# Performance work log

Measured on AMD Instinct MI355X. Metric: run time of the kernel, lower is better.

Reference implementation:

```python
import jax, jax.numpy as jnp
import numpy as np


def _conv(x, w):
    # stride-2, pad-1, 3x3 conv, NCHW activations, HWIO kernel
    return jax.lax.conv_general_dilated(
        x, w, (2, 2), [(1, 1), (1, 1)],
        dimension_numbers=('NCHW', 'HWIO', 'NCHW'))


def setup_inputs() -> dict:
    key = jax.random.key(0)
    ks = iter(jax.random.split(key, 40))
    def rn(shape, scale=1.0):
        return jax.random.normal(next(ks), shape, jnp.float32) * scale
    d = {}
    d['img'] = rn((64, 3, 128, 128))
    d['qst'] = rn((64, 128))
    d['conv_w0'] = rn((3, 3, 3, 24), 1.0 / np.sqrt(3 * 9))
    for i in (1, 2, 3):
        d['conv_w%d' % i] = rn((3, 3, 24, 24), 1.0 / np.sqrt(24 * 9))
    for i in range(4):
        d['bn_s%d' % i] = jax.random.uniform(next(ks), (24,), jnp.float32, 0.5, 1.5)
        d['bn_b%d' % i] = rn((24,), 0.1)
    d['g_w1'] = rn((180, 256), 1.0 / np.sqrt(180))
    d['g_b1'] = rn((256,), 0.01)
    for i in (2, 3, 4):
        d['g_w%d' % i] = rn((256, 256), 1.0 / np.sqrt(256))
        d['g_b%d' % i] = rn((256,), 0.01)
    d['f_w1'] = rn((256, 256), 1.0 / np.sqrt(256))
    d['f_b1'] = rn((256,), 0.01)
    d['f_w2'] = rn((256, 256), 1.0 / np.sqrt(256))
    d['f_b2'] = rn((256,), 0.01)
    d['cls_w'] = rn((256, 32), 1.0 / np.sqrt(256))
    d['cls_b'] = rn((32,), 0.01)
    return d


def reference(img, qst, conv_w0, conv_w1, conv_w2, conv_w3,
              bn_s0, bn_b0, bn_s1, bn_b1, bn_s2, bn_b2, bn_s3, bn_b3,
              g_w1, g_b1, g_w2, g_b2, g_w3, g_b3, g_w4, g_b4,
              f_w1, f_b1, f_w2, f_b2, cls_w, cls_b):
    x = img
    for w, s, b in ((conv_w0, bn_s0, bn_b0), (conv_w1, bn_s1, bn_b1),
                    (conv_w2, bn_s2, bn_b2), (conv_w3, bn_s3, bn_b3)):
        x = jax.nn.relu(_conv(x, w) * s[None, :, None, None] + b[None, :, None, None])
    N, C, H, W = x.shape  # [64, 24, 8, 8]
    # positional encoding: coords_x, coords_y in [-1,1]
    cx, cy = jnp.meshgrid(jnp.linspace(-1.0, 1.0, W), jnp.linspace(-1.0, 1.0, H))
    pos = jnp.broadcast_to(jnp.stack([cx, cy])[None], (N, 2, H, W)).astype(x.dtype)
    x = jnp.concatenate([x, pos], axis=1)              # [N, C+2, H, W]
    Cf = C + 2
    x = x.transpose(0, 2, 3, 1).reshape(N, H * W, Cf)  # [N, HW, 26]
    # RN_G first linear decomposed over concat([x_i, x_j, qst]) so the huge
    # [N, HW, HW, 2C+q] concat tensor is never materialized (same math).
    W1a, W1b, W1c = g_w1[:Cf], g_w1[Cf:2 * Cf], g_w1[2 * Cf:]
    hi = x @ W1a                      # [N, HW, 256]
    hj = x @ W1b                      # [N, HW, 256]
    hq = qst @ W1c + g_b1             # [N, 256]
    h = jax.nn.relu(hi[:, :, None, :] + hj[:, None, :, :] + hq[:, None, None, :])  # [N,HW,HW,256]
    h = jax.nn.relu(h @ g_w2 + g_b2)
    h = jax.nn.relu(h @ g_w3 + g_b3)
    h = jax.nn.relu(h @ g_w4 + g_b4)
    s = h.sum(axis=(1, 2))            # sum over all HW*HW pairs -> [N, 256]
    # RN_F (dropout is identity in eval mode)
    y = jax.nn.relu(s @ f_w1 + f_b1)
    y = jax.nn.relu(y @ f_w2 + f_b2)
    return jax.nn.log_softmax(y @ cls_w + cls_b, axis=1)
```

## Files before the change

### kernel.cpp

```cpp
#include <hip/hip_runtime.h>
#include <hip/hip_bf16.h>
#include <math.h>

typedef __bf16 bf16x8 __attribute__((ext_vector_type(8)));
typedef __bf16 bf16x4 __attribute__((ext_vector_type(4)));
typedef float  f32x4  __attribute__((ext_vector_type(4)));

#define LH 264

__device__ __host__ inline int fperm(int p) {
  return (p & 0xC0) | ((p & 0x0C) << 2) | ((p >> 2) & 0x0C) | (p & 3);
}

__global__ __launch_bounds__(256) void k1(const float* __restrict__ img, const float* __restrict__ w0,
    const float* __restrict__ bs0, const float* __restrict__ bb0,
    const float* __restrict__ g2, const float* __restrict__ g3, const float* __restrict__ g4,
    const float* __restrict__ gw1, const float* __restrict__ gb1, const float* __restrict__ qst,
    float* __restrict__ c0, __bf16* __restrict__ Wt, float* __restrict__ hq,
    float* __restrict__ sbuf) {
  __shared__ __align__(16) float smem[8224];
  const int blk = blockIdx.x, t = threadIdx.x;

  if (blk < 512) {
    float* wl = smem;
    for (int i = t; i < 648; i += 256) wl[i] = w0[i];
    __syncthreads();
    const int H = 128, W = 128, OH = 64, OW = 64;
    int idx = blk * 256 + t;
    int oxh = idx & 31; int tt = idx >> 5; int oy = tt & 63; int n = tt >> 6;
    int ox0 = oxh * 2;
    float acc0[24], acc1[24];
#pragma unroll
    for (int co = 0; co < 24; ++co) { acc0[co] = 0.f; acc1[co] = 0.f; }
    for (int ci = 0; ci < 3; ++ci) {
      const float* xp = img + (size_t)(n * 3 + ci) * H * W;
#pragma unroll
      for (int ky = 0; ky < 3; ++ky) {
        int iy = 2 * oy + ky - 1;
        if (iy < 0 || iy >= H) continue;
        const float* row = xp + (size_t)iy * W;
        int ixb = 2 * ox0 - 1;
        float in[7];
#pragma unroll
        for (int u = 0; u < 7; ++u) {
          int ix = ixb + u;
          in[u] = (ix >= 0 && ix < W) ? row[ix] : 0.f;
        }
#pragma unroll
        for (int kx = 0; kx < 3; ++kx) {
          const float* wp = &wl[((ky * 3 + kx) * 3 + ci) * 24];
          float v0 = in[kx], v1 = in[kx + 2];
#pragma unroll
          for (int co = 0; co < 24; ++co) {
            float wv = wp[co];
            acc0[co] += v0 * wv;
            acc1[co] += v1 * wv;
          }
        }
      }
    }
    float* yp = c0 + (size_t)n * 24 * OH * OW + (size_t)oy * OW + ox0;
#pragma unroll
    for (int co = 0; co < 24; ++co) {
      float s = bs0[co], b = bb0[co];
      yp[(size_t)co * OH * OW]     = fmaxf(acc0[co] * s + b, 0.f);
      yp[(size_t)co * OH * OW + 1] = fmaxf(acc1[co] * s + b, 0.f);
    }
  } else if (blk < 536) {
    float* tile = smem;
    const int lb = blk - 512;
    const int l = lb >> 3, ks = lb & 7;
    const float* src = (l == 0) ? g2 : (l == 1) ? g3 : g4;
    for (int kk = 0; kk < 32; ++kk) tile[kk * 257 + t] = src[(ks * 32 + kk) * 256 + t];
    __syncthreads();
    const int q = t & 3, nb = t >> 2;
    __bf16* out = Wt + (size_t)(l * 8 + ks) * 8192;
#pragma unroll
    for (int i = 0; i < 4; ++i) {
      int nn = i * 64 + nb;
      int fsel = (l < 2) ? fperm(nn) : nn;
      bf16x8 v;
#pragma unroll
      for (int j = 0; j < 8; ++j) v[j] = (__bf16)tile[(q * 8 + j) * 257 + fsel];
      *(bf16x8*)&out[nn * 32 + q * 8] = v;
    }
  } else {
    float* qs = smem;
    const int n = blk - 536;
    sbuf[n * 256 + t] = 0.f;
    if (t < 128) qs[t] = qst[n * 128 + t];
    __syncthreads();
    float a = gb1[t];
    for (int c = 0; c < 128; ++c) a += qs[c] * gw1[(52 + c) * 256 + t];
    hq[n * 256 + t] = a;
  }
}

__global__ __launch_bounds__(256) void conv1_k(const float* __restrict__ x, const float* __restrict__ w,
                                               const float* __restrict__ sc, const float* __restrict__ bi,
                                               float* __restrict__ y) {
  const int H = 64, W = 64, OH = 32, OW = 32;
  __shared__ float wl[2592];
  const int half = blockIdx.x & 1, sb = blockIdx.x >> 1;
  for (int i = threadIdx.x; i < 2592; i += 256) {
    int co = i % 12, rest = i / 12;
    wl[i] = w[rest * 24 + half * 12 + co];
  }
  __syncthreads();

  int idx = sb * 256 + threadIdx.x;
  int oxh = idx & 15; int tt = idx >> 4; int oy = tt & 31; int n = tt >> 5;
  int ox0 = oxh * 2;

  float acc0[12], acc1[12];
#pragma unroll
  for (int co = 0; co < 12; ++co) { acc0[co] = 0.f; acc1[co] = 0.f; }

  for (int ci = 0; ci < 24; ++ci) {
    const float* xp = x + (size_t)(n * 24 + ci) * H * W;
#pragma unroll
    for (int ky = 0; ky < 3; ++ky) {
      int iy = 2 * oy + ky - 1;
      if (iy < 0 || iy >= H) continue;
      const float* row = xp + (size_t)iy * W;
      int ixb = 2 * ox0 - 1;
      float in[7];
#pragma unroll
      for (int u = 0; u < 7; ++u) {
        int ix = ixb + u;
        in[u] = (ix >= 0 && ix < W) ? row[ix] : 0.f;
      }
#pragma unroll
      for (int kx = 0; kx < 3; ++kx) {
        const float* wp = &wl[((ky * 3 + kx) * 24 + ci) * 12];
        float v0 = in[kx], v1 = in[kx + 2];
#pragma unroll
        for (int co = 0; co < 12; ++co) {
          float wv = wp[co];
          acc0[co] += v0 * wv;
          acc1[co] += v1 * wv;
        }
      }
    }
  }
  float* yp = y + (size_t)n * 24 * OH * OW + (size_t)(half * 12) * OH * OW + (size_t)oy * OW + ox0;
#pragma unroll
  for (int co = 0; co < 12; ++co) {
    int cog = half * 12 + co;
    float s = sc[cog], b = bi[cog];
    yp[(size_t)co * OH * OW]     = fmaxf(acc0[co] * s + b, 0.f);
    yp[(size_t)co * OH * OW + 1] = fmaxf(acc1[co] * s + b, 0.f);
  }
}

__global__ __launch_bounds__(256) void chain2_k(const float* __restrict__ c1,
    const float* __restrict__ w2, const float* __restrict__ bs2, const float* __restrict__ bb2,
    const float* __restrict__ w3, const float* __restrict__ bs3, const float* __restrict__ bb3,
    const float* __restrict__ gw1, float* __restrict__ hi, float* __restrict__ hj) {
  __shared__ float sw[5184];
  __shared__ float s2[6144];
  __shared__ float s3[1536];
  const int n = blockIdx.x, t = threadIdx.x;
  for (int i = t; i < 5184; i += 256) sw[i] = w2[i];
  __syncthreads();
  {
    int ox = t & 15, oy = t >> 4;
    float acc[24];
#pragma unroll
    for (int co = 0; co < 24; ++co) acc[co] = 0.f;
    for (int ci = 0; ci < 24; ++ci) {
      const float* xp = c1 + (size_t)(n * 24 + ci) * 1024;
#pragma unroll
      for (int ky = 0; ky < 3; ++ky) {
        int iy = 2 * oy + ky - 1;
        if (iy < 0 || iy >= 32) continue;
#pragma unroll
        for (int kx = 0; kx < 3; ++kx) {
          int ix = 2 * ox + kx - 1;
          if (ix < 0 || ix >= 32) continue;
          float v = xp[iy * 32 + ix];
          const float* wp = &sw[((ky * 3 + kx) * 24 + ci) * 24];
#pragma unroll
          for (int co = 0; co < 24; ++co) acc[co] += v * wp[co];
        }
      }
    }
#pragma unroll
    for (int co = 0; co < 24; ++co)
      s2[co * 256 + t] = fmaxf(acc[co] * bs2[co] + bb2[co], 0.f);
  }
  __syncthreads();
  for (int i = t; i < 5184; i += 256) sw[i] = w3[i];
  __syncthreads();
  {
    const int pos = t & 63, cog = t >> 6;
    const int oy = pos >> 3, ox = pos & 7;
    float acc[6];
#pragma unroll
    for (int u = 0; u < 6; ++u) acc[u] = 0.f;
    for (int ci = 0; ci < 24; ++ci) {
      const float* cp = &s2[ci * 256];
#pragma unroll
      for (int ky = 0; ky < 3; ++ky) {
        int iy = 2 * oy + ky - 1;
        if (iy < 0 || iy >= 16) continue;
#pragma unroll
        for (int kx = 0; kx < 3; ++kx) {
          int ix = 2 * ox + kx - 1;
          if (ix < 0 || ix >= 16) continue;
          float v = cp[iy * 16 + ix];
          const float* wp = &sw[((ky * 3 + kx) * 24 + ci) * 24 + cog * 6];
#pragma unroll
          for (int u = 0; u < 6; ++u) acc[u] += v * wp[u];
        }
      }
    }
#pragma unroll
    for (int u = 0; u < 6; ++u) {
      int co = cog * 6 + u;
      s3[co * 64 + pos] = fmaxf(acc[u] * bs3[co] + bb3[co], 0.f);
    }
  }
  float wa[26], wb[26];
#pragma unroll
  for (int c = 0; c < 26; ++c) {
    wa[c] = gw1[c * 256 + t];
    wb[c] = gw1[(26 + c) * 256 + t];
  }
  __syncthreads();
  for (int p = 0; p < 64; ++p) {
    float a = 0.f, b = 0.f;
#pragma unroll
    for (int c = 0; c < 24; ++c) {
      float v = s3[c * 64 + p];
      a += v * wa[c];
      b += v * wb[c];
    }
    float cx = -1.f + (2.f / 7.f) * (float)(p & 7);
    float cy = -1.f + (2.f / 7.f) * (float)(p >> 3);
    a += cx * wa[24] + cy * wa[25];
    b += cx * wb[24] + cy * wb[25];
    hi[(size_t)(n * 64 + p) * 256 + t] = a;
    hj[(size_t)(n * 64 + p) * 256 + t] = b;
  }
}

__global__ __launch_bounds__(256, 2)
void g_fused(const float* __restrict__ hi, const float* __restrict__ hj,
             const float* __restrict__ hq, const __bf16* __restrict__ Wt,
             const float* __restrict__ b2, const float* __restrict__ b3,
             const float* __restrict__ b4, float* __restrict__ s_out) {
  const int blk = blockIdx.x;
  const int n = blk >> 5, ib = blk & 31;
  const int tid = threadIdx.x;
  const int wave = tid >> 6, lane = tid & 63;
  const int q = lane >> 4, lr = lane & 15;

  __shared__ __align__(16) __bf16 Hs[128 * LH];

  const int half = lane >> 5, m = lane & 31;
  const int cb = m * 8;
  float4 hqA = *(const float4*)(hq + (size_t)n * 256 + cb);
  float4 hqB = *(const float4*)(hq + (size_t)n * 256 + cb + 4);
  float4 hiA = *(const float4*)(hi + (size_t)(n * 64 + ib * 2 + half) * 256 + cb);
  float4 hiB = *(const float4*)(hi + (size_t)(n * 64 + ib * 2 + half) * 256 + cb + 4);
  float hh[8];
  hh[0] = hiA.x + hqA.x; hh[1] = hiA.y + hqA.y; hh[2] = hiA.z + hqA.z; hh[3] = hiA.w + hqA.w;
  hh[4] = hiB.x + hqB.x; hh[5] = hiB.y + hqB.y; hh[6] = hiB.z + hqB.z; hh[7] = hiB.w + hqB.w;

  float bias2[4];
#pragma unroll
  for (int c = 0; c < 4; ++c) bias2[c] = b4[wave * 64 + lr + c * 16];

  const float* hjb = hj + (size_t)n * 64 * 256;
#pragma unroll
  for (int it = 0; it < 16; ++it) {
    int j = it * 4 + wave;
    float4 va = *(const float4*)(hjb + j * 256 + cb);
    float4 vb = *(const float4*)(hjb + j * 256 + cb + 4);
    bf16x8 o;
    o[0] = (__bf16)fmaxf(va.x + hh[0], 0.f);
    o[1] = (__bf16)fmaxf(va.y + hh[1], 0.f);
    o[2] = (__bf16)fmaxf(va.z + hh[2], 0.f);
    o[3] = (__bf16)fmaxf(va.w + hh[3], 0.f);
    o[4] = (__bf16)fmaxf(vb.x + hh[4], 0.f);
    o[5] = (__bf16)fmaxf(vb.y + hh[5], 0.f);
    o[6] = (__bf16)fmaxf(vb.z + hh[6], 0.f);
    o[7] = (__bf16)fmaxf(vb.w + hh[7], 0.f);
    *(bf16x8*)&Hs[(size_t)(half * 64 + j) * LH + cb] = o;
  }
  __syncthreads();

  const __bf16* Bp = Wt + (size_t)wave * 2048 + lr * 32 + q * 8;
  const int colv = wave * 64 + q * 16;

  for (int l = 0; l < 2; ++l) {
    const __bf16* Bl = Bp + (size_t)l * 65536;
    const float* bb = (l == 0) ? b2 : b3;
    f32x4 bv[4];
#pragma unroll
    for (int c = 0; c < 4; ++c)
      bv[c] = *(const f32x4*)(bb + colv + c * 4);

    f32x4 acc[8][4];
#pragma unroll
    for (int r = 0; r < 8; ++r)
#pragma unroll
      for (int c = 0; c < 4; ++c) acc[r][c] = (f32x4){0.f, 0.f, 0.f, 0.f};

    for (int ks = 0; ks < 8; ++ks) {
      bf16x8 b[4];
#pragma unroll
      for (int c = 0; c < 4; ++c)
        b[c] = *(const bf16x8*)&Bl[ks * 8192 + c * 512];
      bf16x8 a[8];
#pragma unroll
      for (int r = 0; r < 8; ++r)
        a[r] = *(const bf16x8*)&Hs[(size_t)(r * 16 + lr) * LH + ks * 32 + q * 8];
#pragma unroll
      for (int r = 0; r < 8; ++r)
#pragma unroll
        for (int c = 0; c < 4; ++c)
          acc[r][c] = __builtin_amdgcn_mfma_f32_16x16x32_bf16(b[c], a[r], acc[r][c], 0, 0, 0);
    }

    __syncthreads();
#pragma unroll
    for (int r = 0; r < 8; ++r) {
      bf16x8 oA, oB;
#pragma unroll
      for (int c = 0; c < 2; ++c)
#pragma unroll
        for (int reg = 0; reg < 4; ++reg)
          oA[c * 4 + reg] = (__bf16)fmaxf(acc[r][c][reg] + bv[c][reg], 0.f);
#pragma unroll
      for (int c = 2; c < 4; ++c)
#pragma unroll
        for (int reg = 0; reg < 4; ++reg)
          oB[(c - 2) * 4 + reg] = (__bf16)fmaxf(acc[r][c][reg] + bv[c][reg], 0.f);
      __bf16* wp = &Hs[(size_t)(r * 16 + lr) * LH + colv];
      *(bf16x8*)wp = oA;
      *(bf16x8*)(wp + 8) = oB;
    }
    __syncthreads();
  }

  {
    const __bf16* Bl = Bp + (size_t)2 * 65536;
    f32x4 acc[8][4];
#pragma unroll
    for (int r = 0; r < 8; ++r)
#pragma unroll
      for (int c = 0; c < 4; ++c) acc[r][c] = (f32x4){0.f, 0.f, 0.f, 0.f};

    for (int ks = 0; ks < 8; ++ks) {
      bf16x8 b[4];
#pragma unroll
      for (int c = 0; c < 4; ++c)
        b[c] = *(const bf16x8*)&Bl[ks * 8192 + c * 512];
      bf16x8 a[8];
#pragma unroll
      for (int r = 0; r < 8; ++r)
        a[r] = *(const bf16x8*)&Hs[(size_t)(r * 16 + lr) * LH + ks * 32 + q * 8];
#pragma unroll
      for (int r = 0; r < 8; ++r)
#pragma unroll
        for (int c = 0; c < 4; ++c)
          acc[r][c] = __builtin_amdgcn_mfma_f32_16x16x32_bf16(a[r], b[c], acc[r][c], 0, 0, 0);
    }

#pragma unroll
    for (int c = 0; c < 4; ++c) {
      float cs = 0.f;
#pragma unroll
      for (int r = 0; r < 8; ++r)
#pragma unroll
        for (int reg = 0; reg < 4; ++reg)
          cs += fmaxf(acc[r][c][reg] + bias2[c], 0.f);
      cs += __shfl_xor(cs, 16);
      cs += __shfl_xor(cs, 32);
      if (q == 0) atomicAdd(&s_out[n * 256 + wave * 64 + lr + c * 16], cs);
    }
  }
}

__global__ void f_net(const float* __restrict__ s, const float* __restrict__ fw1,
                      const float* __restrict__ fb1, const float* __restrict__ fw2,
                      const float* __restrict__ fb2, const float* __restrict__ cw,
                      const float* __restrict__ cb, float* __restrict__ out) {
  int n = blockIdx.x, t = threadIdx.x;
  __shared__ float buf[256], buf2[256], zs[32];
  buf[t] = s[n * 256 + t];
  __syncthreads();
  float a = fb1[t];
  for (int c = 0; c < 256; ++c) a += buf[c] * fw1[c * 256 + t];
  a = fmaxf(a, 0.f);
  buf2[t] = a;
  __syncthreads();
  float y = fb2[t];
  for (int c = 0; c < 256; ++c) y += buf2[c] * fw2[c * 256 + t];
  y = fmaxf(y, 0.f);
  __syncthreads();
  buf[t] = y;
  __syncthreads();
  float z = 0.f;
  if (t < 32) {
    z = cb[t];
    for (int c = 0; c < 256; ++c) z += buf[c] * cw[c * 32 + t];
    zs[t] = z;
  }
  __syncthreads();
  if (t < 32) {
    float m = -1e30f;
    for (int c = 0; c < 32; ++c) m = fmaxf(m, zs[c]);
    float se = 0.f;
    for (int c = 0; c < 32; ++c) se += expf(zs[c] - m);
    out[n * 32 + t] = z - m - logf(se);
  }
}

extern "C" void kernel_launch(void* const* d_in, const int* in_sizes, int n_in,
                              void* d_out, int out_size, void* d_ws, size_t ws_size,
                              hipStream_t stream) {
  const float* img  = (const float*)d_in[0];
  const float* qst  = (const float*)d_in[1];
  const float* w0   = (const float*)d_in[2];
  const float* w1   = (const float*)d_in[3];
  const float* w2   = (const float*)d_in[4];
  const float* w3   = (const float*)d_in[5];
  const float* bs0  = (const float*)d_in[6];
  const float* bb0  = (const float*)d_in[7];
  const float* bs1  = (const float*)d_in[8];
  const float* bb1  = (const float*)d_in[9];
  const float* bs2  = (const float*)d_in[10];
  const float* bb2  = (const float*)d_in[11];
  const float* bs3  = (const float*)d_in[12];
  const float* bb3  = (const float*)d_in[13];
  const float* gw1  = (const float*)d_in[14];
  const float* gb1  = (const float*)d_in[15];
  const float* gw2  = (const float*)d_in[16];
  const float* gb2  = (const float*)d_in[17];
  const float* gw3  = (const float*)d_in[18];
  const float* gb3  = (const float*)d_in[19];
  const float* gw4  = (const float*)d_in[20];
  const float* gb4  = (const float*)d_in[21];
  const float* fw1  = (const float*)d_in[22];
  const float* fb1  = (const float*)d_in[23];
  const float* fw2  = (const float*)d_in[24];
  const float* fb2  = (const float*)d_in[25];
  const float* cw   = (const float*)d_in[26];
  const float* cb   = (const float*)d_in[27];

  char* ws = (char*)d_ws;
  float* c0 = (float*)(ws + 0);
  float* c1 = (float*)(ws + 25165824);
  __bf16* Wt  = (__bf16*)(ws + 31457280);
  float*  hqb = (float*)(ws + 31850496);
  float*  sbuf = (float*)(ws + 31916032);
  float*  hi  = (float*)(ws + 0);
  float*  hj  = (float*)(ws + 4194304);

  k1<<<600, 256, 0, stream>>>(img, w0, bs0, bb0, gw2, gw3, gw4, gw1, gb1, qst,
                              c0, Wt, hqb, sbuf);
  conv1_k<<<256, 256, 0, stream>>>(c0, w1, bs1, bb1, c1);
  chain2_k<<<64, 256, 0, stream>>>(c1, w2, bs2, bb2, w3, bs3, bb3, gw1, hi, hj);
  g_fused<<<2048, 256, 0, stream>>>(hi, hj, hqb, Wt, gb2, gb3, gb4, sbuf);
  f_net<<<64, 256, 0, stream>>>(sbuf, fw1, fb1, fw2, fb2, cw, cb, (float*)d_out);
}
```

Before: 308.9 us.

## Prefetch MFMA B operands, raise MFMA priority, retile conv1 and unroll f_net

```diff
diff --git a/kernel.cpp b/kernel.cpp
--- a/kernel.cpp
+++ b/kernel.cpp
@@ -34,22 +34,24 @@
     for (int co = 0; co < 24; ++co) { acc0[co] = 0.f; acc1[co] = 0.f; }
     for (int ci = 0; ci < 3; ++ci) {
       const float* xp = img + (size_t)(n * 3 + ci) * H * W;
+      float in[3][7];
 #pragma unroll
       for (int ky = 0; ky < 3; ++ky) {
         int iy = 2 * oy + ky - 1;
-        if (iy < 0 || iy >= H) continue;
+        bool yok = (iy >= 0) && (iy < H);
         const float* row = xp + (size_t)iy * W;
-        int ixb = 2 * ox0 - 1;
-        float in[7];
 #pragma unroll
         for (int u = 0; u < 7; ++u) {
-          int ix = ixb + u;
-          in[u] = (ix >= 0 && ix < W) ? row[ix] : 0.f;
+          int ix = 2 * ox0 - 1 + u;
+          in[ky][u] = (yok && ix >= 0 && ix < W) ? row[ix] : 0.f;
         }
+      }
+#pragma unroll
+      for (int ky = 0; ky < 3; ++ky)
 #pragma unroll
         for (int kx = 0; kx < 3; ++kx) {
           const float* wp = &wl[((ky * 3 + kx) * 3 + ci) * 24];
-          float v0 = in[kx], v1 = in[kx + 2];
+          float v0 = in[ky][kx], v1 = in[ky][kx + 2];
 #pragma unroll
           for (int co = 0; co < 24; ++co) {
             float wv = wp[co];
@@ -57,7 +59,6 @@
             acc1[co] += v1 * wv;
           }
         }
-      }
     }
     float* yp = c0 + (size_t)n * 24 * OH * OW + (size_t)oy * OW + ox0;
 #pragma unroll
@@ -109,12 +110,11 @@
   __syncthreads();
 
   int idx = sb * 256 + threadIdx.x;
-  int oxh = idx & 15; int tt = idx >> 4; int oy = tt & 31; int n = tt >> 5;
-  int ox0 = oxh * 2;
-
-  float acc0[12], acc1[12];
-#pragma unroll
-  for (int co = 0; co < 12; ++co) { acc0[co] = 0.f; acc1[co] = 0.f; }
+  int ox = idx & 31, oy = (idx >> 5) & 31, n = idx >> 10;
+
+  float acc[12];
+#pragma unroll
+  for (int co = 0; co < 12; ++co) acc[co] = 0.f;
 
   for (int ci = 0; ci < 24; ++ci) {
     const float* xp = x + (size_t)(n * 24 + ci) * H * W;
@@ -123,33 +123,26 @@
       int iy = 2 * oy + ky - 1;
       if (iy < 0 || iy >= H) continue;
       const float* row = xp + (size_t)iy * W;
-      int ixb = 2 * ox0 - 1;
-      float in[7];
-#pragma unroll
-      for (int u = 0; u < 7; ++u) {
-        int ix = ixb + u;
+      float in[3];
+#pragma unroll
+      for (int u = 0; u < 3; ++u) {
+        int ix = 2 * ox - 1 + u;
         in[u] = (ix >= 0 && ix < W) ? row[ix] : 0.f;
       }
 #pragma unroll
       for (int kx = 0; kx < 3; ++kx) {
         const float* wp = &wl[((ky * 3 + kx) * 24 + ci) * 12];
-        float v0 = in[kx], v1 = in[kx + 2];
-#pragma unroll
-        for (int co = 0; co < 12; ++co) {
-          float wv = wp[co];
-          acc0[co] += v0 * wv;
-          acc1[co] += v1 * wv;
-        }
-      }
-    }
-  }
-  float* yp = y + (size_t)n * 24 * OH * OW + (size_t)(half * 12) * OH * OW + (size_t)oy * OW + ox0;
+        float v = in[kx];
+#pragma unroll
+        for (int co = 0; co < 12; ++co) acc[co] += v * wp[co];
+      }
+    }
+  }
+  float* yp = y + (size_t)(n * 24 + half * 12) * OH * OW + (size_t)oy * OW + ox;
 #pragma unroll
   for (int co = 0; co < 12; ++co) {
     int cog = half * 12 + co;
-    float s = sc[cog], b = bi[cog];
-    yp[(size_t)co * OH * OW]     = fmaxf(acc0[co] * s + b, 0.f);
-    yp[(size_t)co * OH * OW + 1] = fmaxf(acc1[co] * s + b, 0.f);
+    yp[(size_t)co * OH * OW] = fmaxf(acc[co] * sc[cog] + bi[cog], 0.f);
   }
 }
 
@@ -308,20 +301,29 @@
 #pragma unroll
       for (int c = 0; c < 4; ++c) acc[r][c] = (f32x4){0.f, 0.f, 0.f, 0.f};
 
+    bf16x8 bnxt[4];
+#pragma unroll
+    for (int c = 0; c < 4; ++c) bnxt[c] = *(const bf16x8*)&Bl[c * 512];
+#pragma unroll
     for (int ks = 0; ks < 8; ++ks) {
-      bf16x8 b[4];
-#pragma unroll
-      for (int c = 0; c < 4; ++c)
-        b[c] = *(const bf16x8*)&Bl[ks * 8192 + c * 512];
+      bf16x8 bcur[4];
+#pragma unroll
+      for (int c = 0; c < 4; ++c) bcur[c] = bnxt[c];
+      if (ks < 7) {
+#pragma unroll
+        for (int c = 0; c < 4; ++c) bnxt[c] = *(const bf16x8*)&Bl[(ks + 1) * 8192 + c * 512];
+      }
       bf16x8 a[8];
 #pragma unroll
       for (int r = 0; r < 8; ++r)
         a[r] = *(const bf16x8*)&Hs[(size_t)(r * 16 + lr) * LH + ks * 32 + q * 8];
+      __builtin_amdgcn_s_setprio(1);
 #pragma unroll
       for (int r = 0; r < 8; ++r)
 #pragma unroll
         for (int c = 0; c < 4; ++c)
-          acc[r][c] = __builtin_amdgcn_mfma_f32_16x16x32_bf16(b[c], a[r], acc[r][c], 0, 0, 0);
+          acc[r][c] = __builtin_amdgcn_mfma_f32_16x16x32_bf16(bcur[c], a[r], acc[r][c], 0, 0, 0);
+      __builtin_amdgcn_s_setprio(0);
     }
 
     __syncthreads();
@@ -353,20 +355,29 @@
 #pragma unroll
       for (int c = 0; c < 4; ++c) acc[r][c] = (f32x4){0.f, 0.f, 0.f, 0.f};
 
+    bf16x8 bnxt[4];
+#pragma unroll
+    for (int c = 0; c < 4; ++c) bnxt[c] = *(const bf16x8*)&Bl[c * 512];
+#pragma unroll
     for (int ks = 0; ks < 8; ++ks) {
-      bf16x8 b[4];
-#pragma unroll
-      for (int c = 0; c < 4; ++c)
-        b[c] = *(const bf16x8*)&Bl[ks * 8192 + c * 512];
+      bf16x8 bcur[4];
+#pragma unroll
+      for (int c = 0; c < 4; ++c) bcur[c] = bnxt[c];
+      if (ks < 7) {
+#pragma unroll
+        for (int c = 0; c < 4; ++c) bnxt[c] = *(const bf16x8*)&Bl[(ks + 1) * 8192 + c * 512];
+      }
       bf16x8 a[8];
 #pragma unroll
       for (int r = 0; r < 8; ++r)
         a[r] = *(const bf16x8*)&Hs[(size_t)(r * 16 + lr) * LH + ks * 32 + q * 8];
+      __builtin_amdgcn_s_setprio(1);
 #pragma unroll
       for (int r = 0; r < 8; ++r)
 #pragma unroll
         for (int c = 0; c < 4; ++c)
-          acc[r][c] = __builtin_amdgcn_mfma_f32_16x16x32_bf16(a[r], b[c], acc[r][c], 0, 0, 0);
+          acc[r][c] = __builtin_amdgcn_mfma_f32_16x16x32_bf16(a[r], bcur[c], acc[r][c], 0, 0, 0);
+      __builtin_amdgcn_s_setprio(0);
     }
 
 #pragma unroll
@@ -392,30 +403,46 @@
   __shared__ float buf[256], buf2[256], zs[32];
   buf[t] = s[n * 256 + t];
   __syncthreads();
-  float a = fb1[t];
-  for (int c = 0; c < 256; ++c) a += buf[c] * fw1[c * 256 + t];
-  a = fmaxf(a, 0.f);
+  float a0 = 0.f, a1 = 0.f, a2 = 0.f, a3 = 0.f;
+  for (int c = 0; c < 256; c += 4) {
+    a0 += buf[c]     * fw1[c * 256 + t];
+    a1 += buf[c + 1] * fw1[(c + 1) * 256 + t];
+    a2 += buf[c + 2] * fw1[(c + 2) * 256 + t];
+    a3 += buf[c + 3] * fw1[(c + 3) * 256 + t];
+  }
+  float a = fmaxf(fb1[t] + ((a0 + a1) + (a2 + a3)), 0.f);
   buf2[t] = a;
   __syncthreads();
-  float y = fb2[t];
-  for (int c = 0; c < 256; ++c) y += buf2[c] * fw2[c * 256 + t];
-  y = fmaxf(y, 0.f);
+  float y0 = 0.f, y1 = 0.f, y2 = 0.f, y3 = 0.f;
+  for (int c = 0; c < 256; c += 4) {
+    y0 += buf2[c]     * fw2[c * 256 + t];
+    y1 += buf2[c + 1] * fw2[(c + 1) * 256 + t];
+    y2 += buf2[c + 2] * fw2[(c + 2) * 256 + t];
+    y3 += buf2[c + 3] * fw2[(c + 3) * 256 + t];
+  }
+  float y = fmaxf(fb2[t] + ((y0 + y1) + (y2 + y3)), 0.f);
   __syncthreads();
   buf[t] = y;
   __syncthreads();
   float z = 0.f;
   if (t < 32) {
-    z = cb[t];
-    for (int c = 0; c < 256; ++c) z += buf[c] * cw[c * 32 + t];
+    float z0 = 0.f, z1 = 0.f, z2 = 0.f, z3 = 0.f;
+    for (int c = 0; c < 256; c += 4) {
+      z0 += buf[c]     * cw[c * 32 + t];
+      z1 += buf[c + 1] * cw[(c + 1) * 32 + t];
+      z2 += buf[c + 2] * cw[(c + 2) * 32 + t];
+      z3 += buf[c + 3] * cw[(c + 3) * 32 + t];
+    }
+    z = cb[t] + ((z0 + z1) + (z2 + z3));
     zs[t] = z;
   }
   __syncthreads();
   if (t < 32) {
-    float m = -1e30f;
-    for (int c = 0; c < 32; ++c) m = fmaxf(m, zs[c]);
+    float mx = -1e30f;
+    for (int c = 0; c < 32; ++c) mx = fmaxf(mx, zs[c]);
     float se = 0.f;
-    for (int c = 0; c < 32; ++c) se += expf(zs[c] - m);
-    out[n * 32 + t] = z - m - logf(se);
+    for (int c = 0; c < 32; ++c) se += expf(zs[c] - mx);
+    out[n * 32 + t] = z - mx - logf(se);
   }
 }
 
@@ -462,7 +489,7 @@
 
   k1<<<600, 256, 0, stream>>>(img, w0, bs0, bb0, gw2, gw3, gw4, gw1, gb1, qst,
                               c0, Wt, hqb, sbuf);
-  conv1_k<<<256, 256, 0, stream>>>(c0, w1, bs1, bb1, c1);
+  conv1_k<<<512, 256, 0, stream>>>(c0, w1, bs1, bb1, c1);
   chain2_k<<<64, 256, 0, stream>>>(c1, w2, bs2, bb2, w3, bs3, bb3, gw1, hi, hj);
   g_fused<<<2048, 256, 0, stream>>>(hi, hj, hqb, Wt, gb2, gb3, gb4, sbuf);
   f_net<<<64, 256, 0, stream>>>(sbuf, fw1, fb1, fw2, fb2, cw, cb, (float*)d_out);
```

After: 307.9 us. About the same (-0.3%).
